# Optimization experiments

Hardware: AMD Instinct MI355X
Metric: run time of the kernel (lower is better)

Reference implementation:

```python
import jax, jax.numpy as jnp
import numpy as np

# ---- architecture constants (from init_kwargs / arch_args) ----
IN_BITS, IN_FRAC, BITS_PER_STREAM = 8, 4, 2
N_STREAMS = IN_BITS // BITS_PER_STREAM          # 4
W_BITS, BITS_PER_SLICE = 8, 2
N_SLICES = W_BITS // BITS_PER_SLICE             # 4
ADC_BITS = 5
ADC_MAX = 2.0 ** ADC_BITS - 1.0                 # 31
SUBARRAY_SIZE = 128
IC, OC, K, STRIDE, PAD = 64, 64, 3, 1, 1
F_TOTAL = IC * K * K                            # 576 unfolded features
N_SUB = (F_TOTAL + SUBARRAY_SIZE - 1) // SUBARRAY_SIZE  # 5 subarrays
CHUNK = -(-F_TOTAL // N_SUB)                    # 116, matches torch.chunk sizes


def bit_stream(x):
    """VectorizedInputBitStreaming.forward: fixed-point quantize + two's complement + bit-serial split."""
    int_bits = IN_BITS - IN_FRAC - 1
    max_val = 2.0 ** int_bits - 2.0 ** (-IN_FRAC)
    q = jnp.round(jnp.clip(x, -(2.0 ** int_bits), max_val) * (2 ** IN_FRAC)).astype(jnp.int32)
    q = jnp.where(q < 0, (1 << IN_BITS) + q, q)  # two's complement encode
    shifts = jnp.arange(0, IN_BITS, BITS_PER_STREAM, dtype=jnp.int32)
    return ((q[..., None] >> shifts) & ((1 << BITS_PER_STREAM) - 1)).astype(jnp.float32)


def bit_slice(w):
    """VectorizedWeightBitSlicing.forward: pos/neg split, normalize by max abs, integer bit-slice."""
    wp = jnp.maximum(w, 0.0)
    wn = jnp.maximum(-w, 0.0)
    max_abs = jnp.maximum(wp.max(), wn.max())
    max_abs = jnp.where(max_abs > 0, max_abs, 1.0)
    mv = 2 ** W_BITS - 1
    pi = jnp.round(wp / max_abs * mv).astype(jnp.int32)
    ni = jnp.round(wn / max_abs * mv).astype(jnp.int32)
    shifts = jnp.arange(0, W_BITS, BITS_PER_SLICE, dtype=jnp.int32)
    mask = (1 << BITS_PER_SLICE) - 1
    pos = ((pi[..., None] >> shifts) & mask).astype(jnp.float32)
    neg = ((ni[..., None] >> shifts) & mask).astype(jnp.float32)
    return pos, neg, max_abs


def adc(x):
    """Nbit_ADC simulated: uniform round + clip to [0, 2^adc_bits - 1]."""
    return jnp.clip(jnp.round(x), 0.0, ADC_MAX)


def _forward(inputs, weight):
    # unfold -> (B, IC*K*K, H', W') with (c, kh, kw)-major feature ordering like F.unfold
    patches = jax.lax.conv_general_dilated_patches(
        inputs, (K, K), (STRIDE, STRIDE), [(PAD, PAD), (PAD, PAD)])
    B, F, H, W = patches.shape
    P = H * W
    patches = patches.reshape(B, F, P)

    streams = bit_stream(patches)                     # (B, F, P, S)
    pos_sl, neg_sl, norm = bit_slice(weight)
    pos_m = pos_sl.reshape(OC, F, N_SLICES)           # (O, F, T)
    neg_m = neg_sl.reshape(OC, F, N_SLICES)

    # zero-pad feature dim to N_SUB*CHUNK and reshape into subarray chunks
    pad = N_SUB * CHUNK - F
    streams = jnp.pad(streams, ((0, 0), (0, pad), (0, 0), (0, 0))).reshape(B, N_SUB, CHUNK, P, N_STREAMS)
    pos_m = jnp.pad(pos_m, ((0, 0), (0, pad), (0, 0))).reshape(OC, N_SUB, CHUNK, N_SLICES)
    neg_m = jnp.pad(neg_m, ((0, 0), (0, pad), (0, 0))).reshape(OC, N_SUB, CHUNK, N_SLICES)

    # per-subarray analog MAC: (c, b, o, p, s, t)
    pos_r = jnp.einsum('bcfps,ocft->cbopst', streams, pos_m)
    neg_r = jnp.einsum('bcfps,ocft->cbopst', streams, neg_m)

    # ADC quantize, then weight by 2^(stream*bits) * 2^(slice*bits), sum over s,t and subarrays c
    scale = (2.0 ** (jnp.arange(N_STREAMS) * BITS_PER_STREAM))[:, None] * \
            (2.0 ** (jnp.arange(N_SLICES) * BITS_PER_SLICE))[None, :]
    diff = jnp.einsum('cbopst,st->bop', adc(pos_r) - adc(neg_r), scale)

    out = diff * norm / (2.0 ** IN_BITS - 1.0)
    return out.reshape(B, OC, H, W), jnp.float32(0.0)


def setup_inputs() -> dict:
    key = jax.random.key(0)
    k1, k2 = jax.random.split(key)
    inputs = jax.random.normal(k1, (4, IC, 32, 32), dtype=jnp.float32)
    # kaiming_normal_-like init
    weight = jax.random.normal(k2, (OC, IC, K, K), dtype=jnp.float32) * (2.0 / (IC * K * K)) ** 0.5
    return {"inputs": inputs, "weight": weight}


def reference(inputs, weight):
    return _forward(inputs, weight)
```

## Files before the change

### kernel.cpp

```cpp
#include <hip/hip_runtime.h>
#include <stdint.h>


typedef int v4i __attribute__((ext_vector_type(4)));
typedef unsigned int v4u __attribute__((ext_vector_type(4)));

#define BROW 656

__device__ __forceinline__ v4i bits2(v4u w, int s) {
  v4u r = (w >> (unsigned)(2 * s)) & 0x03030303u;
  return (v4i)r;
}

__global__ __launch_bounds__(256) void k_fused(
    const float* __restrict__ in, const float* __restrict__ w,
    float* __restrict__ out)
{
  __shared__ unsigned char Al[32 * BROW];
  __shared__ unsigned char Bl[64 * BROW];
  __shared__ float s_part[4];

  int tid = threadIdx.x;
  int bid = blockIdx.x;
  if (bid == 0 && tid == 0) out[262144] = 0.0f;

  int mtile = bid >> 1;
  int ohalf = bid & 1;

  #pragma unroll
  for (int i = 0; i < 5; ++i) {
    int idx = i * 256 + tid;
    int loc = idx >> 2, dw = idx & 3;
    int sign = loc >= 160 ? 1 : 0;
    int r = loc - sign * 160;
    unsigned int o_l = ((unsigned)r * 52429u) >> 18;
    int c = r - (int)o_l * 5;
    ((unsigned int*)Bl)[(sign * 32 + (int)o_l) * 164 + c * 32 + 28 + dw] = 0u;
  }

  {
    int b = mtile >> 5;
    int pbase = (mtile & 31) * 32;
    #pragma unroll 2
    for (int i = 0; i < 20; ++i) {
      int d = i * 256 + tid;
      unsigned int m_l = ((unsigned)d * 52429u) >> 23;
      int kw = d - (int)m_l * 160;
      int p = pbase + (int)m_l;
      int y = p >> 5, x = p & 31;
      unsigned int pack = 0;
      #pragma unroll
      for (int q = 0; q < 4; ++q) {
        int k = kw * 4 + q;
        int c = k >> 7, j = k & 127;
        int csize = (c == 4) ? 112 : 116;
        unsigned int bv = 0;
        if (j < csize) {
          unsigned int f  = c * 116 + j;
          unsigned int ic = (f * 7282u) >> 16;
          unsigned int r9 = f - ic * 9u;
          unsigned int dy = (r9 * 11u) >> 5;
          unsigned int dx = r9 - dy * 3u;
          int iy = y + (int)dy - 1, ix = x + (int)dx - 1;
          if (iy >= 0 && iy < 32 && ix >= 0 && ix < 32) {
            float xv = in[((b * 64 + (int)ic) * 32 + iy) * 32 + ix];
            xv = fminf(fmaxf(xv, -8.0f), 7.9375f);
            bv = (unsigned int)((int)rintf(xv * 16.0f) & 255);
          }
        }
        pack |= bv << (8 * q);
      }
      ((unsigned int*)Al)[(int)m_l * 164 + kw] = pack;
    }
  }

  {
    const float4* w4 = (const float4*)w;
    float a = 0.0f;
    #pragma unroll 4
    for (int i = 0; i < 36; ++i) {
      float4 v = w4[i * 256 + tid];
      a = fmaxf(a, fmaxf(fmaxf(fabsf(v.x), fabsf(v.y)),
                         fmaxf(fabsf(v.z), fabsf(v.w))));
    }
    #pragma unroll
    for (int off = 32; off > 0; off >>= 1)
      a = fmaxf(a, __shfl_down(a, off, 64));
    if ((tid & 63) == 0) s_part[tid >> 6] = a;
  }
  __syncthreads();

  float norm = fmaxf(fmaxf(s_part[0], s_part[1]), fmaxf(s_part[2], s_part[3]));
  if (!(norm > 0.0f)) norm = 1.0f;
  float sc = 255.0f / norm;

  #pragma unroll 2
  for (int i = 0; i < 18; ++i) {
    int idx = i * 256 + tid;
    unsigned int o_l = (((unsigned)idx >> 4) * 7282u) >> 16;
    int g = idx - (int)o_l * 144;
    int c, jg;
    if (g < 116) { c = (g * 565) >> 14; jg = (g - c * 29) * 4; }
    else         { c = 4;               jg = (g - 116) * 4; }
    int f = c * 116 + jg;
    float4 wv = *(const float4*)(w + (ohalf * 32 + (int)o_l) * 576 + f);
    float vv[4] = {wv.x, wv.y, wv.z, wv.w};
    unsigned int pd = 0, nd = 0;
    #pragma unroll
    for (int q = 0; q < 4; ++q) {
      unsigned int pb = (unsigned int)(int)rintf(fmaxf(vv[q], 0.0f) * sc);
      unsigned int nb = (unsigned int)(int)rintf(fmaxf(-vv[q], 0.0f) * sc);
      pd |= pb << (8 * q);
      nd |= nb << (8 * q);
    }
    int dwo = c * 32 + (jg >> 2);
    ((unsigned int*)Bl)[((int)o_l) * 164 + dwo]       = pd;
    ((unsigned int*)Bl)[(32 + (int)o_l) * 164 + dwo]  = nd;
  }
  __syncthreads();

  int lane = tid & 63, wave = tid >> 6;
  int msub = wave >> 1, osub = wave & 1;
  int r16 = lane & 15, kgrp = lane >> 4;

  const unsigned char* ap = Al + (msub * 16 + r16) * BROW + kgrp * 16;
  const unsigned char* bp = Bl + (osub * 16 + r16) * BROW + kgrp * 16;
  const unsigned char* bn = Bl + (32 + osub * 16 + r16) * BROW + kgrp * 16;

  v4i outacc = {0, 0, 0, 0};

  #pragma unroll
  for (int c = 0; c < 5; ++c) {
    v4u a0 = *(const v4u*)(ap + c * 128);
    v4u a1 = *(const v4u*)(ap + c * 128 + 64);
    v4u p0 = *(const v4u*)(bp + c * 128);
    v4u p1 = *(const v4u*)(bp + c * 128 + 64);
    v4u n0 = *(const v4u*)(bn + c * 128);
    v4u n1 = *(const v4u*)(bn + c * 128 + 64);

    v4i btp0[4], btp1[4], btn0[4], btn1[4];
    #pragma unroll
    for (int t = 0; t < 4; ++t) {
      btp0[t] = bits2(p0, t); btp1[t] = bits2(p1, t);
      btn0[t] = bits2(n0, t); btn1[t] = bits2(n1, t);
    }

    #pragma unroll
    for (int s = 0; s < 4; ++s) {
      v4i as0 = bits2(a0, s), as1 = bits2(a1, s);
      #pragma unroll
      for (int t = 0; t < 4; ++t) {
        v4i z = {0, 0, 0, 0};
        v4i pacc = __builtin_amdgcn_mfma_i32_16x16x64_i8(btp0[t], as0, z, 0, 0, 0);
        pacc     = __builtin_amdgcn_mfma_i32_16x16x64_i8(btp1[t], as1, pacc, 0, 0, 0);
        v4i nacc = __builtin_amdgcn_mfma_i32_16x16x64_i8(btn0[t], as0, z, 0, 0, 0);
        nacc     = __builtin_amdgcn_mfma_i32_16x16x64_i8(btn1[t], as1, nacc, 0, 0, 0);
        int sh = 2 * (s + t);
        #pragma unroll
        for (int r = 0; r < 4; ++r) {
          int d = (pacc[r] < 31 ? pacc[r] : 31) - (nacc[r] < 31 ? nacc[r] : 31);
          outacc[r] += d << sh;
        }
      }
    }
  }

  float fsc = norm / 255.0f;
  int m = mtile * 32 + msub * 16 + r16;
  int b = m >> 10, p = m & 1023;
  int oc = ohalf * 32 + osub * 16 + kgrp * 4;
  #pragma unroll
  for (int r = 0; r < 4; ++r)
    out[(b * 64 + oc + r) * 1024 + p] = (float)outacc[r] * fsc;
}

extern "C" void kernel_launch(void* const* d_in, const int* in_sizes, int n_in,
                              void* d_out, int out_size, void* d_ws, size_t ws_size,
                              hipStream_t stream) {
  const float* inp = (const float*)d_in[0];
  const float* wgt = (const float*)d_in[1];
  float* out = (float*)d_out;
  (void)d_ws; (void)ws_size;
  k_fused<<<256, 256, 0, stream>>>(inp, wgt, out);
}
```

Baseline: 88.62 us.

## Split work across input bit-streams per wave and double grid size

Launches 512 blocks of 512 threads, each block covering one output row of 32 pixels and 16 output channels. Each of the 8 waves handles one input bit-stream s for one 16-row half, with results reduced through shared memory at the end. The weight max-abs load is issued before the input staging to overlap its latency. This trades redundant per-block staging of the input patch and full weight-max scan (twice as many blocks) plus an extra reduction barrier for more parallelism and less MFMA work per wave.

```diff
diff --git a/kernel.cpp b/kernel.cpp
--- a/kernel.cpp
+++ b/kernel.cpp
@@ -5,49 +5,57 @@
 typedef int v4i __attribute__((ext_vector_type(4)));
 typedef unsigned int v4u __attribute__((ext_vector_type(4)));
 
-#define BROW 656
+#define BROW  656
+#define BROWD 164
 
 __device__ __forceinline__ v4i bits2(v4u w, int s) {
   v4u r = (w >> (unsigned)(2 * s)) & 0x03030303u;
   return (v4i)r;
 }
 
-__global__ __launch_bounds__(256) void k_fused(
+__global__ __launch_bounds__(512, 4) void k_fused(
     const float* __restrict__ in, const float* __restrict__ w,
     float* __restrict__ out)
 {
-  __shared__ unsigned char Al[32 * BROW];
-  __shared__ unsigned char Bl[64 * BROW];
-  __shared__ float s_part[4];
+  __shared__ __align__(16) unsigned char Al[32 * BROW];
+  __shared__ __align__(16) unsigned char Bl[32 * BROW];
+  __shared__ float s_part[8];
 
   int tid = threadIdx.x;
   int bid = blockIdx.x;
   if (bid == 0 && tid == 0) out[262144] = 0.0f;
 
-  int mtile = bid >> 1;
-  int ohalf = bid & 1;
+  int mtile = bid >> 2;
+  int otile = bid & 3;
 
-  #pragma unroll
-  for (int i = 0; i < 5; ++i) {
-    int idx = i * 256 + tid;
-    int loc = idx >> 2, dw = idx & 3;
-    int sign = loc >= 160 ? 1 : 0;
-    int r = loc - sign * 160;
-    unsigned int o_l = ((unsigned)r * 52429u) >> 18;
-    int c = r - (int)o_l * 5;
-    ((unsigned int*)Bl)[(sign * 32 + (int)o_l) * 164 + c * 32 + 28 + dw] = 0u;
+  float amax = 0.0f;
+  {
+    const float4* w4 = (const float4*)w;
+    #pragma unroll 6
+    for (int i = 0; i < 18; ++i) {
+      float4 v = w4[i * 512 + tid];
+      amax = fmaxf(amax, fmaxf(fmaxf(fabsf(v.x), fabsf(v.y)),
+                               fmaxf(fabsf(v.z), fabsf(v.w))));
+    }
+  }
+
+  {
+    int row  = tid >> 4;
+    int slot = tid & 15;
+    int c, dw;
+    if (slot < 12) { c = (slot * 11) >> 5; dw = 29 + slot - c * 3; }
+    else           { c = 4;                dw = slot + 16; }
+    ((unsigned int*)Bl)[row * BROWD + c * 32 + dw] = 0u;
   }
 
   {
     int b = mtile >> 5;
-    int pbase = (mtile & 31) * 32;
+    int yrow = mtile & 31;
     #pragma unroll 2
-    for (int i = 0; i < 20; ++i) {
-      int d = i * 256 + tid;
+    for (int i = 0; i < 10; ++i) {
+      int d = i * 512 + tid;
       unsigned int m_l = ((unsigned)d * 52429u) >> 23;
       int kw = d - (int)m_l * 160;
-      int p = pbase + (int)m_l;
-      int y = p >> 5, x = p & 31;
       unsigned int pack = 0;
       #pragma unroll
       for (int q = 0; q < 4; ++q) {
@@ -61,7 +69,7 @@
           unsigned int r9 = f - ic * 9u;
           unsigned int dy = (r9 * 11u) >> 5;
           unsigned int dx = r9 - dy * 3u;
-          int iy = y + (int)dy - 1, ix = x + (int)dx - 1;
+          int iy = yrow + (int)dy - 1, ix = (int)m_l + (int)dx - 1;
           if (iy >= 0 && iy < 32 && ix >= 0 && ix < 32) {
             float xv = in[((b * 64 + (int)ic) * 32 + iy) * 32 + ix];
             xv = fminf(fmaxf(xv, -8.0f), 7.9375f);
@@ -70,62 +78,56 @@
         }
         pack |= bv << (8 * q);
       }
-      ((unsigned int*)Al)[(int)m_l * 164 + kw] = pack;
+      ((unsigned int*)Al)[m_l * BROWD + kw] = pack;
     }
   }
 
-  {
-    const float4* w4 = (const float4*)w;
-    float a = 0.0f;
-    #pragma unroll 4
-    for (int i = 0; i < 36; ++i) {
-      float4 v = w4[i * 256 + tid];
-      a = fmaxf(a, fmaxf(fmaxf(fabsf(v.x), fabsf(v.y)),
-                         fmaxf(fabsf(v.z), fabsf(v.w))));
-    }
-    #pragma unroll
-    for (int off = 32; off > 0; off >>= 1)
-      a = fmaxf(a, __shfl_down(a, off, 64));
-    if ((tid & 63) == 0) s_part[tid >> 6] = a;
-  }
+  #pragma unroll
+  for (int off = 32; off > 0; off >>= 1)
+    amax = fmaxf(amax, __shfl_down(amax, off, 64));
+  if ((tid & 63) == 0) s_part[tid >> 6] = amax;
   __syncthreads();
 
-  float norm = fmaxf(fmaxf(s_part[0], s_part[1]), fmaxf(s_part[2], s_part[3]));
+  float norm = s_part[0];
+  #pragma unroll
+  for (int i = 1; i < 8; ++i) norm = fmaxf(norm, s_part[i]);
   if (!(norm > 0.0f)) norm = 1.0f;
   float sc = 255.0f / norm;
 
-  #pragma unroll 2
-  for (int i = 0; i < 18; ++i) {
-    int idx = i * 256 + tid;
-    unsigned int o_l = (((unsigned)idx >> 4) * 7282u) >> 16;
-    int g = idx - (int)o_l * 144;
-    int c, jg;
-    if (g < 116) { c = (g * 565) >> 14; jg = (g - c * 29) * 4; }
-    else         { c = 4;               jg = (g - 116) * 4; }
-    int f = c * 116 + jg;
-    float4 wv = *(const float4*)(w + (ohalf * 32 + (int)o_l) * 576 + f);
-    float vv[4] = {wv.x, wv.y, wv.z, wv.w};
-    unsigned int pd = 0, nd = 0;
-    #pragma unroll
-    for (int q = 0; q < 4; ++q) {
-      unsigned int pb = (unsigned int)(int)rintf(fmaxf(vv[q], 0.0f) * sc);
-      unsigned int nb = (unsigned int)(int)rintf(fmaxf(-vv[q], 0.0f) * sc);
-      pd |= pb << (8 * q);
-      nd |= nb << (8 * q);
+  #pragma unroll
+  for (int i = 0; i < 5; ++i) {
+    int idx = i * 512 + tid;
+    if (idx < 2304) {
+      unsigned int o_l = ((unsigned)idx * 1821u) >> 18;
+      int g = idx - (int)o_l * 144;
+      int c, jg;
+      if (g < 116) { c = (g * 565) >> 14; jg = (g - c * 29) * 4; }
+      else         { c = 4;               jg = (g - 116) * 4; }
+      int f = c * 116 + jg;
+      float4 wv = *(const float4*)(w + (otile * 16 + (int)o_l) * 576 + f);
+      float vv[4] = {wv.x, wv.y, wv.z, wv.w};
+      unsigned int pd = 0, nd = 0;
+      #pragma unroll
+      for (int q = 0; q < 4; ++q) {
+        unsigned int pb = (unsigned int)(int)rintf(fmaxf(vv[q], 0.0f) * sc);
+        unsigned int nb = (unsigned int)(int)rintf(fmaxf(-vv[q], 0.0f) * sc);
+        pd |= pb << (8 * q);
+        nd |= nb << (8 * q);
+      }
+      int dwo = c * 32 + (jg >> 2);
+      ((unsigned int*)Bl)[(int)o_l * BROWD + dwo]        = pd;
+      ((unsigned int*)Bl)[(16 + (int)o_l) * BROWD + dwo] = nd;
     }
-    int dwo = c * 32 + (jg >> 2);
-    ((unsigned int*)Bl)[((int)o_l) * 164 + dwo]       = pd;
-    ((unsigned int*)Bl)[(32 + (int)o_l) * 164 + dwo]  = nd;
   }
   __syncthreads();
 
   int lane = tid & 63, wave = tid >> 6;
-  int msub = wave >> 1, osub = wave & 1;
+  int s = wave & 3, msub = wave >> 2;
   int r16 = lane & 15, kgrp = lane >> 4;
 
   const unsigned char* ap = Al + (msub * 16 + r16) * BROW + kgrp * 16;
-  const unsigned char* bp = Bl + (osub * 16 + r16) * BROW + kgrp * 16;
-  const unsigned char* bn = Bl + (32 + osub * 16 + r16) * BROW + kgrp * 16;
+  const unsigned char* bp = Bl + r16 * BROW + kgrp * 16;
+  const unsigned char* bn = Bl + (16 + r16) * BROW + kgrp * 16;
 
   v4i outacc = {0, 0, 0, 0};
 
@@ -138,40 +140,42 @@
     v4u n0 = *(const v4u*)(bn + c * 128);
     v4u n1 = *(const v4u*)(bn + c * 128 + 64);
 
-    v4i btp0[4], btp1[4], btn0[4], btn1[4];
+    v4i as0 = bits2(a0, s), as1 = bits2(a1, s);
+
     #pragma unroll
     for (int t = 0; t < 4; ++t) {
-      btp0[t] = bits2(p0, t); btp1[t] = bits2(p1, t);
-      btn0[t] = bits2(n0, t); btn1[t] = bits2(n1, t);
-    }
-
-    #pragma unroll
-    for (int s = 0; s < 4; ++s) {
-      v4i as0 = bits2(a0, s), as1 = bits2(a1, s);
+      v4i z = {0, 0, 0, 0};
+      v4i pacc = __builtin_amdgcn_mfma_i32_16x16x64_i8(bits2(p0, t), as0, z, 0, 0, 0);
+      pacc     = __builtin_amdgcn_mfma_i32_16x16x64_i8(bits2(p1, t), as1, pacc, 0, 0, 0);
+      v4i nacc = __builtin_amdgcn_mfma_i32_16x16x64_i8(bits2(n0, t), as0, z, 0, 0, 0);
+      nacc     = __builtin_amdgcn_mfma_i32_16x16x64_i8(bits2(n1, t), as1, nacc, 0, 0, 0);
+      int sh = 2 * (s + t);
       #pragma unroll
-      for (int t = 0; t < 4; ++t) {
-        v4i z = {0, 0, 0, 0};
-        v4i pacc = __builtin_amdgcn_mfma_i32_16x16x64_i8(btp0[t], as0, z, 0, 0, 0);
-        pacc     = __builtin_amdgcn_mfma_i32_16x16x64_i8(btp1[t], as1, pacc, 0, 0, 0);
-        v4i nacc = __builtin_amdgcn_mfma_i32_16x16x64_i8(btn0[t], as0, z, 0, 0, 0);
-        nacc     = __builtin_amdgcn_mfma_i32_16x16x64_i8(btn1[t], as1, nacc, 0, 0, 0);
-        int sh = 2 * (s + t);
-        #pragma unroll
-        for (int r = 0; r < 4; ++r) {
-          int d = (pacc[r] < 31 ? pacc[r] : 31) - (nacc[r] < 31 ? nacc[r] : 31);
-          outacc[r] += d << sh;
-        }
+      for (int r = 0; r < 4; ++r) {
+        int dd = (pacc[r] < 31 ? pacc[r] : 31) - (nacc[r] < 31 ? nacc[r] : 31);
+        outacc[r] += dd << sh;
       }
     }
   }
 
-  float fsc = norm / 255.0f;
-  int m = mtile * 32 + msub * 16 + r16;
-  int b = m >> 10, p = m & 1023;
-  int oc = ohalf * 32 + osub * 16 + kgrp * 4;
-  #pragma unroll
-  for (int r = 0; r < 4; ++r)
-    out[(b * 64 + oc + r) * 1024 + p] = (float)outacc[r] * fsc;
+  __syncthreads();
+  v4i* red = (v4i*)Al;
+  red[wave * 64 + lane] = outacc;
+  __syncthreads();
+
+  if (s == 0) {
+    v4i acc = red[(msub * 4 + 0) * 64 + lane];
+    #pragma unroll
+    for (int ss = 1; ss < 4; ++ss)
+      acc += red[(msub * 4 + ss) * 64 + lane];
+    float fsc = norm / 255.0f;
+    int pg = mtile * 32 + msub * 16 + r16;
+    int b = pg >> 10, p = pg & 1023;
+    int oc = otile * 16 + kgrp * 4;
+    #pragma unroll
+    for (int r = 0; r < 4; ++r)
+      out[(b * 64 + oc + r) * 1024 + p] = (float)acc[r] * fsc;
+  }
 }
 
 extern "C" void kernel_launch(void* const* d_in, const int* in_sizes, int n_in,
@@ -181,5 +185,5 @@
   const float* wgt = (const float*)d_in[1];
   float* out = (float*)d_out;
   (void)d_ws; (void)ws_size;
-  k_fused<<<256, 256, 0, stream>>>(inp, wgt, out);
+  k_fused<<<512, 512, 0, stream>>>(inp, wgt, out);
 }
```

Result: no change. 88.96 us (+0.4%).
